# Performance work log

Hardware: AMD Instinct MI355X
Metric: run time of the kernel (lower is better)

## Reference

```python
import jax, jax.numpy as jnp
import numpy as np

B, H, W = 4, 112, 112
N = H * W              # 12544 tokens
NBHD = 48              # local neighborhood size
DIM = 256
OUT_DIM = 512
INNER = 4              # inner_ch of weight_net
TABLE = 4096           # pre_table rows
ALPHA = 4.0
DS_RATE = 0.25
STRIDE = 2
RESERVE = (H // 4) * (W // 4)  # 784 reserve tokens (pos % 4 == 0)
EPS = 1e-5


def _ln(x, g, b):
    m = x.mean(-1, keepdims=True)
    v = ((x - m) ** 2).mean(-1, keepdims=True)
    return (x - m) / jnp.sqrt(v + EPS) * g + b


def setup_inputs() -> dict:
    key = jax.random.key(0)
    ks = jax.random.split(key, 8)
    ii, jj = jnp.meshgrid(jnp.arange(H), jnp.arange(W), indexing='ij')
    pos = jnp.stack([ii, jj], -1).reshape(1, N, 2).astype(jnp.float32)
    pos = jnp.tile(pos, (B, 1, 1))                             # b x n x 2 integer grid
    feat = jax.random.normal(ks[0], (B, N, DIM), jnp.float32)
    member_idx = jax.random.randint(ks[1], (B, N, NBHD), 0, N)
    cluster_mask = (jax.random.uniform(ks[2], (B, N, NBHD)) > 0.1).astype(jnp.float32)
    learned_prob = jax.random.uniform(ks[3], (B, N, 1), dtype=jnp.float32)
    pe_idx = jax.random.randint(ks[4], (B, N, NBHD), 0, TABLE)
    pre_table = jax.random.normal(ks[5], (TABLE, 5), jnp.float32)
    w1 = jax.random.normal(ks[6], (5, INNER), jnp.float32) * 0.4
    b1 = jnp.zeros((INNER,), jnp.float32)
    ln1_g = jnp.ones((INNER,), jnp.float32)
    ln1_b = jnp.zeros((INNER,), jnp.float32)
    norm_g = jnp.ones((INNER * DIM,), jnp.float32)
    norm_b = jnp.zeros((INNER * DIM,), jnp.float32)
    lin_w = jax.random.normal(ks[7], (INNER * DIM, OUT_DIM), jnp.float32) * (1.0 / np.sqrt(INNER * DIM))
    lin_b = jnp.zeros((OUT_DIM,), jnp.float32)
    return dict(pos=pos, feat=feat, member_idx=member_idx, cluster_mask=cluster_mask,
                learned_prob=learned_prob, stride=STRIDE, pe_idx=pe_idx, reserve_num=RESERVE,
                pre_table=pre_table, w1=w1, b1=b1, ln1_g=ln1_g, ln1_b=ln1_b,
                norm_g=norm_g, norm_b=norm_b, lin_w=lin_w, lin_b=lin_b)


def reference(pos, feat, member_idx, cluster_mask, learned_prob, stride, pe_idx,
              reserve_num, pre_table, w1, b1, ln1_g, ln1_b, norm_g, norm_b, lin_w, lin_b):
    b, n, c = feat.shape
    keep_num = int(n * DS_RATE)
    pos_long = pos.astype(jnp.int32)
    # stride == 2 branch: tokens on the coarse grid get prob 1
    grid_prob = jnp.all(pos_long % stride == 0, axis=-1).astype(jnp.float32)      # b x n
    lp_s = jax.lax.stop_gradient(learned_prob).reshape(b, n) * ALPHA              # detached scores
    final_prob = grid_prob + lp_s
    reserve_mask = jnp.all(pos_long % (stride * 2) == 0, axis=-1).astype(jnp.float32)
    final_prob = final_prob + reserve_mask * (-100.0)
    sample_num = keep_num - reserve_num
    _, sample_idx = jax.lax.top_k(final_prob, sample_num)                         # b x sample_num
    # per-row nonzero of reserve_mask (exactly reserve_num hits per row)
    flat_nz = jnp.nonzero(reserve_mask.reshape(-1) > 0, size=b * reserve_num)[0]
    reserve_idx = (flat_nz % n).reshape(b, reserve_num).astype(sample_idx.dtype)
    idx = jnp.concatenate([sample_idx, reserve_idx], axis=1)                      # b x keep_num

    pos_k = jnp.take_along_axis(pos, idx[:, :, None], axis=1)                     # b x keep x 2
    nbhd = member_idx.shape[-1]
    mem_k = jnp.take_along_axis(member_idx, idx[:, :, None], axis=1)              # b x keep x nbhd
    pe_k = jnp.take_along_axis(pe_idx, idx[:, :, None], axis=1)
    cm_k = jnp.take_along_axis(cluster_mask, idx[:, :, None], axis=1)
    lp = jnp.take_along_axis(learned_prob, mem_k.reshape(b, -1, 1), axis=1)
    lp = lp.reshape(b, keep_num, nbhd, 1)

    # weight_net on the small PE table, then gather per-edge weights
    wt = jax.nn.gelu(_ln(pre_table @ w1 + b1, ln1_g, ln1_b), approximate=False)   # TABLE x INNER
    weights = wt[pe_k]                                                            # b x keep x nbhd x INNER
    weights = weights * (lp * cm_k[..., None])

    # CLUSTENWF: gather neighbor features and weighted-sum over the neighborhood
    gathered = jnp.take_along_axis(feat, mem_k.reshape(b, -1, 1), axis=1)
    gathered = gathered.reshape(b, keep_num, nbhd, c)                             # b x keep x nbhd x c
    out = jnp.einsum('bnkm,bnkc->bnmc', weights, gathered).reshape(b, keep_num, INNER * c)
    out = _ln(out, norm_g, norm_b)
    return pos_k, out @ lin_w + lin_b
```

## Files before the change

### kernel.cpp

```cpp
#include <hip/hip_runtime.h>

typedef unsigned short u16;
typedef unsigned int u32;
typedef unsigned long long u64;

#define NB 4
#define NTOK 12544
#define NBHD 48
#define DIM 256
#define OUTD 512
#define KEEPN 3136
#define SAMPLEN 2352
#define RESN 784
#define GW 112
#define POSN (NB * KEEPN * 2)
#define QTR (NTOK / 4)
#define NBKT 16384

#define BLKM 128
#define BLKN 256
#define BROW 40

#define FEATB_BYTES (25690112ull)
#define XWS_BYTES   (25690112ull)
#define LINT_BYTES  (1048576ull)
#define KEYS_BYTES  (401408ull)
#define PART_BYTES  (802816ull)
#define WS_NEED (FEATB_BYTES + XWS_BYTES + LINT_BYTES + KEYS_BYTES + PART_BYTES)

__device__ __forceinline__ float bf2f(u16 u) {
    union { u32 i; float f; } v; v.i = ((u32)u) << 16; return v.f;
}
__device__ __forceinline__ float asf(u32 u) {
    union { u32 i; float f; } v; v.i = u; return v.f;
}
__device__ __forceinline__ u16 f2bf(float f) {
    union { u32 i; float f; } v; v.f = f;
    return (u16)((v.i + 0x7FFFu + ((v.i >> 16) & 1u)) >> 16);
}

typedef __bf16 bf16x8 __attribute__((ext_vector_type(8)));
typedef float floatx4 __attribute__((ext_vector_type(4)));

__device__ __forceinline__ float make_f(float lp, int n) {
    int i = n / GW, j = n % GW;
    float f = lp * 4.0f;
    if (((i | j) & 1) == 0) f = 1.0f + f;
    if (((i | j) & 3) == 0) f = f + (-100.0f);
    return f;
}
__device__ __forceinline__ u64 f_to_key(float f, int n) {
    union { float f; u32 u; } v; v.f = f;
    u32 m = (v.u & 0x80000000u) ? ~v.u : (v.u | 0x80000000u);
    return (((u64)m) << 32) | (u64)(0xFFFFFFFFu - (u32)n);
}
__device__ __forceinline__ int f_to_bucket(float f) {
    int b = (int)floorf(f * 3276.8f);
    return b < 0 ? 0 : (b > NBKT - 1 ? NBKT - 1 : b);
}

__global__ __launch_bounds__(256) void feat_cvt_kernel(
    const float* __restrict__ feat, u16* __restrict__ featb) {
    int t = blockIdx.x * 256 + threadIdx.x;
    float4 v = ((const float4*)feat)[t];
    u64 w = (u64)f2bf(v.x) | ((u64)f2bf(v.y) << 16) |
            ((u64)f2bf(v.z) << 32) | ((u64)f2bf(v.w) << 48);
    ((u64*)featb)[t] = w;
}

__global__ __launch_bounds__(256) void linT_cvt_kernel(
    const float* __restrict__ lin_w, u16* __restrict__ linT,
    u32* __restrict__ hist) {
    __shared__ u16 T[64 * 65];
    int k0 = blockIdx.x * 64, n0 = blockIdx.y * 64;
    int t = threadIdx.x;
    int bid = blockIdx.y * 16 + blockIdx.x;
    hist[bid * 512 + t] = 0;
    hist[bid * 512 + 256 + t] = 0;
    int r = t >> 2, c4 = (t & 3) * 16;
#pragma unroll
    for (int i = 0; i < 4; ++i) {
        float4 v = *(const float4*)&lin_w[(size_t)(k0 + r) * OUTD + n0 + c4 + i * 4];
        T[(c4 + i * 4 + 0) * 65 + r] = f2bf(v.x);
        T[(c4 + i * 4 + 1) * 65 + r] = f2bf(v.y);
        T[(c4 + i * 4 + 2) * 65 + r] = f2bf(v.z);
        T[(c4 + i * 4 + 3) * 65 + r] = f2bf(v.w);
    }
    __syncthreads();
    int nl = t >> 2, kc = (t & 3) * 16;
    union { uint4 v[2]; u16 h[16]; } u;
#pragma unroll
    for (int i = 0; i < 16; ++i) u.h[i] = T[nl * 65 + kc + i];
    u16* dst = &linT[(size_t)(n0 + nl) * 1024 + k0 + kc];
    *(uint4*)(dst + 0) = u.v[0];
    *(uint4*)(dst + 8) = u.v[1];
}

__global__ __launch_bounds__(256) void hist_kernel(
    const float* __restrict__ lprob, u32* __restrict__ hist) {
    int g = blockIdx.x * 256 + threadIdx.x;
    int b = g / NTOK, n = g % NTOK;
    int bkt = f_to_bucket(make_f(lprob[g], n));
    atomicAdd(&hist[b * NBKT + bkt], 1u);
}

__global__ __launch_bounds__(1024) void prefix_kernel(
    const u32* __restrict__ hist, u32* __restrict__ base, u32* __restrict__ cursor) {
    int b = blockIdx.x, t = threadIdx.x;
    const u32* h = hist + b * NBKT;
    u32 loc[16], own = 0;
#pragma unroll
    for (int i = 0; i < 16; ++i) { loc[i] = h[t * 16 + i]; own += loc[i]; }
    __shared__ u32 buf[2][1024];
    buf[0][t] = own;
    __syncthreads();
    int src = 0;
    for (int off = 1; off < 1024; off <<= 1) {
        u32 v = buf[src][t] + ((t + off < 1024) ? buf[src][t + off] : 0u);
        buf[src ^ 1][t] = v;
        src ^= 1;
        __syncthreads();
    }
    u32 above = buf[src][t] - own;
    u32 suf = 0, bout[16];
    for (int i = 15; i >= 0; --i) { bout[i] = above + suf; suf += loc[i]; }
    u32* bb = base + b * NBKT;
    u32* cc = cursor + b * NBKT;
#pragma unroll
    for (int i = 0; i < 16; ++i) { bb[t * 16 + i] = bout[i]; cc[t * 16 + i] = bout[i]; }
}

__global__ __launch_bounds__(256) void scatter_kernel(
    const float* __restrict__ lprob, u32* __restrict__ cursor,
    u64* __restrict__ slots) {
    int g = blockIdx.x * 256 + threadIdx.x;
    int b = g / NTOK, n = g % NTOK;
    float f = make_f(lprob[g], n);
    int bkt = f_to_bucket(f);
    u32 s = atomicAdd(&cursor[b * NBKT + bkt], 1u);
    slots[b * NTOK + s] = f_to_key(f, n);
}

__global__ __launch_bounds__(256) void rank_finalize_kernel(
    const float* __restrict__ lprob, const u32* __restrict__ hist,
    const u32* __restrict__ base, const u64* __restrict__ slots,
    float* __restrict__ pos_out) {
    int g = blockIdx.x * 256 + threadIdx.x;
    int b = g / NTOK, n = g % NTOK;
    int i = n / GW, j = n % GW;
    if (((i | j) & 3) == 0) {
        int r = (i >> 2) * 28 + (j >> 2);
        int slot = b * KEEPN + SAMPLEN + r;
        pos_out[slot * 2 + 0] = (float)i;
        pos_out[slot * 2 + 1] = (float)j;
        return;
    }
    float f = make_f(lprob[g], n);
    int bkt = f_to_bucket(f);
    u32 r0 = base[b * NBKT + bkt];
    if (r0 >= SAMPLEN) return;
    u64 my = f_to_key(f, n);
    u32 cnt = hist[b * NBKT + bkt];
    const u64* sl = slots + b * NTOK + r0;
    u32 rank = r0;
    for (u32 s = 0; s < cnt; ++s) rank += (sl[s] > my) ? 1u : 0u;
    if (rank < SAMPLEN) {
        int slot = b * KEEPN + (int)rank;
        pos_out[slot * 2 + 0] = (float)i;
        pos_out[slot * 2 + 1] = (float)j;
    }
}

#define PSTR 20
__global__ __launch_bounds__(256) void token_v2_kernel(
    const float* __restrict__ pos_in, u16* __restrict__ xdst,
    const int* __restrict__ member_idx, const int* __restrict__ pe_idx,
    const float* __restrict__ cmask, const float* __restrict__ lprob,
    const u16* __restrict__ featb, const float* __restrict__ pre_table,
    const float* __restrict__ w1, const float* __restrict__ b1,
    const float* __restrict__ g1, const float* __restrict__ bb1,
    const float* __restrict__ norm_g, const float* __restrict__ norm_b) {
    int bi = blockIdx.x;
    int xcd = bi & 7, jj = bi >> 3;
    int b = xcd >> 1;
    int t = b * KEEPN + (xcd & 1) * 1568 + jj;
    int tid = threadIdx.x;
    int wave = tid >> 6, lane = tid & 63;
    __shared__ int mem_s[NBHD];
    __shared__ float4 w_s[NBHD];
    __shared__ float partials[4 * 64 * PSTR];
    __shared__ float red[10];

    int n_src = (int)pos_in[t * 2 + 0] * GW + (int)pos_in[t * 2 + 1];

    if (tid < NBHD) {
        int e = (b * NTOK + n_src) * NBHD + tid;
        int mem = member_idx[e];
        int pe = pe_idx[e];
        float cm = cmask[e];
        float lpe = lprob[b * NTOK + mem];
        float z[4];
#pragma unroll
        for (int m = 0; m < 4; ++m) {
            float acc = b1[m];
#pragma unroll
            for (int d = 0; d < 5; ++d) acc += pre_table[pe * 5 + d] * w1[d * 4 + m];
            z[m] = acc;
        }
        float mean = (z[0] + z[1] + z[2] + z[3]) * 0.25f;
        float var = 0.0f;
#pragma unroll
        for (int m = 0; m < 4; ++m) { float d = z[m] - mean; var += d * d; }
        float rstd = rsqrtf(var * 0.25f + 1e-5f);
        float sc = lpe * cm;
        float wv[4];
#pragma unroll
        for (int m = 0; m < 4; ++m) {
            float y = (z[m] - mean) * rstd * g1[m] + bb1[m];
            wv[m] = 0.5f * y * (1.0f + erff(y * 0.70710678118654752f)) * sc;
        }
        w_s[tid] = make_float4(wv[0], wv[1], wv[2], wv[3]);
        mem_s[tid] = mem;
    }
    __syncthreads();

    float acc[16];
#pragma unroll
    for (int i = 0; i < 16; ++i) acc[i] = 0.0f;
    const u16* fbase = featb + (size_t)b * NTOK * DIM + lane * 4;
    int k0 = wave * 12;
#pragma unroll
    for (int kk = 0; kk < 12; ++kk) {
        int k = k0 + kk;
        uint2 d = *(const uint2*)(fbase + (size_t)mem_s[k] * DIM);
        float4 w = w_s[k];
        float c0 = asf(d.x << 16);
        float c1 = asf(d.x & 0xFFFF0000u);
        float c2 = asf(d.y << 16);
        float c3 = asf(d.y & 0xFFFF0000u);
        acc[0]  += w.x * c0; acc[1]  += w.y * c0; acc[2]  += w.z * c0; acc[3]  += w.w * c0;
        acc[4]  += w.x * c1; acc[5]  += w.y * c1; acc[6]  += w.z * c1; acc[7]  += w.w * c1;
        acc[8]  += w.x * c2; acc[9]  += w.y * c2; acc[10] += w.z * c2; acc[11] += w.w * c2;
        acc[12] += w.x * c3; acc[13] += w.y * c3; acc[14] += w.z * c3; acc[15] += w.w * c3;
    }
    float* pp = &partials[(wave * 64 + lane) * PSTR];
#pragma unroll
    for (int i = 0; i < 4; ++i)
        *(float4*)(pp + i * 4) = make_float4(acc[i * 4], acc[i * 4 + 1],
                                             acc[i * 4 + 2], acc[i * 4 + 3]);
    __syncthreads();

    int c = tid;
    float a[4] = {0.f, 0.f, 0.f, 0.f};
#pragma unroll
    for (int w = 0; w < 4; ++w) {
        float4 v = *(const float4*)&partials[(w * 64 + (c >> 2)) * PSTR + (c & 3) * 4];
        a[0] += v.x; a[1] += v.y; a[2] += v.z; a[3] += v.w;
    }

    float s1 = a[0] + a[1] + a[2] + a[3];
    float s2 = a[0] * a[0] + a[1] * a[1] + a[2] * a[2] + a[3] * a[3];
#pragma unroll
    for (int off = 32; off > 0; off >>= 1) {
        s1 += __shfl_down(s1, off, 64);
        s2 += __shfl_down(s2, off, 64);
    }
    if (lane == 0) { red[wave] = s1; red[4 + wave] = s2; }
    __syncthreads();
    if (tid == 0) {
        float S = red[0] + red[1] + red[2] + red[3];
        float Q = red[4] + red[5] + red[6] + red[7];
        float mean = S * (1.0f / 1024.0f);
        float var = fmaxf(Q * (1.0f / 1024.0f) - mean * mean, 0.0f);
        red[8] = mean; red[9] = rsqrtf(var + 1e-5f);
    }
    __syncthreads();
    float mean = red[8], rstd = red[9];
    u16* Xp = xdst + (size_t)t * 1024;
#pragma unroll
    for (int m = 0; m < 4; ++m) {
        int cc = m * 256 + c;
        float v = (a[m] - mean) * rstd * norm_g[cc] + norm_b[cc];
        Xp[cc] = f2bf(v);
    }
}

#define GROW 40
__global__ __launch_bounds__(256) void gemm_tile_kernel(
    const u16* __restrict__ xws, const u16* __restrict__ linT,
    const float* __restrict__ lin_b, float* __restrict__ out) {
    __shared__ __align__(16) u16 As[128 * GROW];
    __shared__ __align__(16) u16 Bs[128 * GROW];
    int tid = threadIdx.x;
    int wave = tid >> 6, lane = tid & 63;
    int l15 = lane & 15, quad = lane >> 4;
    int wm = wave >> 1, wn = wave & 1;
    int m0 = blockIdx.x * 128, n0 = blockIdx.y * 128;
    int sr = tid >> 2, sk = (tid & 3) * 8;

    const u16* Ap0 = xws + (size_t)(m0 + sr) * 1024 + sk;
    const u16* Ap1 = Ap0 + (size_t)64 * 1024;
    const u16* Bp0 = linT + (size_t)(n0 + sr) * 1024 + sk;
    const u16* Bp1 = Bp0 + (size_t)64 * 1024;

    floatx4 acc[4][4] = {};
    for (int kk = 0; kk < 1024; kk += 32) {
        uint4 a0 = *(const uint4*)(Ap0 + kk);
        uint4 a1 = *(const uint4*)(Ap1 + kk);
        uint4 b0 = *(const uint4*)(Bp0 + kk);
        uint4 b1 = *(const uint4*)(Bp1 + kk);
        __syncthreads();
        *(uint4*)&As[sr * GROW + sk] = a0;
        *(uint4*)&As[(64 + sr) * GROW + sk] = a1;
        *(uint4*)&Bs[sr * GROW + sk] = b0;
        *(uint4*)&Bs[(64 + sr) * GROW + sk] = b1;
        __syncthreads();
        bf16x8 af[4], bfv[4];
#pragma unroll
        for (int mi = 0; mi < 4; ++mi)
            af[mi] = *(const bf16x8*)&As[(wm * 64 + mi * 16 + l15) * GROW + quad * 8];
#pragma unroll
        for (int ni = 0; ni < 4; ++ni)
            bfv[ni] = *(const bf16x8*)&Bs[(wn * 64 + ni * 16 + l15) * GROW + quad * 8];
#pragma unroll
        for (int mi = 0; mi < 4; ++mi)
#pragma unroll
            for (int ni = 0; ni < 4; ++ni)
                acc[mi][ni] = __builtin_amdgcn_mfma_f32_16x16x32_bf16(
                    af[mi], bfv[ni], acc[mi][ni], 0, 0, 0);
    }
#pragma unroll
    for (int ni = 0; ni < 4; ++ni) {
        int col = n0 + wn * 64 + ni * 16 + l15;
        float bias = lin_b[col];
#pragma unroll
        for (int mi = 0; mi < 4; ++mi)
#pragma unroll
            for (int reg = 0; reg < 4; ++reg) {
                int row = m0 + wm * 64 + mi * 16 + quad * 4 + reg;
                out[(size_t)row * OUTD + col] = acc[mi][ni][reg] + bias;
            }
    }
}

__global__ __launch_bounds__(256) void key_kernel(
    const float* __restrict__ lprob, u64* __restrict__ keys) {
    int g = blockIdx.x * 256 + threadIdx.x;
    int n = g % NTOK;
    keys[g] = f_to_key(make_f(lprob[g], n), n);
}

__global__ __launch_bounds__(256) void partial_rank_kernel(
    const u64* __restrict__ keys, u32* __restrict__ part) {
    int b = blockIdx.y, z = blockIdx.z;
    int n = blockIdx.x * 256 + threadIdx.x;
    u64 my = keys[b * NTOK + n];
    const u64* kb = keys + b * NTOK + z * QTR;
    u32 cnt = 0;
    for (int t = 0; t < QTR; t += 8) {
#pragma unroll
        for (int j = 0; j < 8; ++j) cnt += (kb[t + j] > my) ? 1u : 0u;
    }
    part[(z * NB + b) * NTOK + n] = cnt;
}

__global__ __launch_bounds__(256) void finalize_kernel(
    const u32* __restrict__ part, float* __restrict__ pos_out) {
    int b = blockIdx.y;
    int n = blockIdx.x * 256 + threadIdx.x;
    int g = b * NTOK + n;
    u32 rank = part[g] + part[(NB + b) * NTOK + n] +
               part[(2 * NB + b) * NTOK + n] + part[(3 * NB + b) * NTOK + n];
    int i = n / GW, j = n % GW;
    if (rank < SAMPLEN) {
        int slot = b * KEEPN + (int)rank;
        pos_out[slot * 2 + 0] = (float)i;
        pos_out[slot * 2 + 1] = (float)j;
    }
    if (((i | j) & 3) == 0) {
        int r = (i >> 2) * 28 + (j >> 2);
        int slot = b * KEEPN + SAMPLEN + r;
        pos_out[slot * 2 + 0] = (float)i;
        pos_out[slot * 2 + 1] = (float)j;
    }
}

__global__ __launch_bounds__(256) void token_fb_kernel(
    const float* __restrict__ pos_in, u16* __restrict__ xdst,
    const int* __restrict__ member_idx, const int* __restrict__ pe_idx,
    const float* __restrict__ cmask, const float* __restrict__ lprob,
    const float* __restrict__ featf, const float* __restrict__ pre_table,
    const float* __restrict__ w1, const float* __restrict__ b1,
    const float* __restrict__ g1, const float* __restrict__ bb1,
    const float* __restrict__ norm_g, const float* __restrict__ norm_b) {
    int t = blockIdx.x;
    int b = t / KEEPN;
    int tid = threadIdx.x;
    __shared__ int mem_s[NBHD];
    __shared__ float4 w_s[NBHD];
    __shared__ float red[10];

    int n_src = (int)pos_in[t * 2 + 0] * GW + (int)pos_in[t * 2 + 1];

    if (tid < NBHD) {
        int e = (b * NTOK + n_src) * NBHD + tid;
        int mem = member_idx[e];
        int pe = pe_idx[e];
        float cm = cmask[e];
        float lpe = lprob[b * NTOK + mem];
        float z[4];
#pragma unroll
        for (int m = 0; m < 4; ++m) {
            float acc = b1[m];
#pragma unroll
            for (int d = 0; d < 5; ++d) acc += pre_table[pe * 5 + d] * w1[d * 4 + m];
            z[m] = acc;
        }
        float mean = (z[0] + z[1] + z[2] + z[3]) * 0.25f;
        float var = 0.0f;
#pragma unroll
        for (int m = 0; m < 4; ++m) { float d = z[m] - mean; var += d * d; }
        float rstd = rsqrtf(var * 0.25f + 1e-5f);
        float sc = lpe * cm;
        float wv[4];
#pragma unroll
        for (int m = 0; m < 4; ++m) {
            float y = (z[m] - mean) * rstd * g1[m] + bb1[m];
            wv[m] = 0.5f * y * (1.0f + erff(y * 0.70710678118654752f)) * sc;
        }
        w_s[tid] = make_float4(wv[0], wv[1], wv[2], wv[3]);
        mem_s[tid] = mem;
    }
    __syncthreads();

    float a0 = 0.f, a1 = 0.f, a2 = 0.f, a3 = 0.f;
    size_t base = (size_t)b * NTOK * DIM + tid;
#pragma unroll 8
    for (int k = 0; k < NBHD; ++k) {
        float g = featf[base + (size_t)mem_s[k] * DIM];
        float4 w = w_s[k];
        a0 += w.x * g; a1 += w.y * g; a2 += w.z * g; a3 += w.w * g;
    }
    float s1 = a0 + a1 + a2 + a3;
    float s2 = a0 * a0 + a1 * a1 + a2 * a2 + a3 * a3;
#pragma unroll
    for (int off = 32; off > 0; off >>= 1) {
        s1 += __shfl_down(s1, off, 64);
        s2 += __shfl_down(s2, off, 64);
    }
    int wave = tid >> 6, lane = tid & 63;
    if (lane == 0) { red[wave] = s1; red[4 + wave] = s2; }
    __syncthreads();
    if (tid == 0) {
        float S = red[0] + red[1] + red[2] + red[3];
        float Q = red[4] + red[5] + red[6] + red[7];
        float mean = S * (1.0f / 1024.0f);
        float var = fmaxf(Q * (1.0f / 1024.0f) - mean * mean, 0.0f);
        red[8] = mean; red[9] = rsqrtf(var + 1e-5f);
    }
    __syncthreads();
    float mean = red[8], rstd = red[9];
    float acc4[4] = {a0, a1, a2, a3};
    u16* Xp = xdst + (size_t)t * 1024;
#pragma unroll
    for (int m = 0; m < 4; ++m) {
        int cc = m * 256 + tid;
        float v = (acc4[m] - mean) * rstd * norm_g[cc] + norm_b[cc];
        Xp[cc] = f2bf(v);
    }
}

__global__ __launch_bounds__(256) void gemm_inplace_kernel(
    const float* __restrict__ lin_w, const float* __restrict__ lin_b,
    float* __restrict__ out) {
    __shared__ __align__(16) u16 Bs[BLKN * BROW];
    int tile_m = blockIdx.x;
    int nblk = blockIdx.y;
    int tid = threadIdx.x;
    int wave = tid >> 6, lane = tid & 63;
    int l15 = lane & 15, quad = lane >> 4;

    const u16* Xbase = (const u16*)out;
    floatx4 acc[8][4] = {};

    for (int kk = 0; kk < 1024; kk += 32) {
        __syncthreads();
#pragma unroll
        for (int it = 0; it < 4; ++it) {
            int task = it * 256 + tid;
            int kp = task >> 6;
            int ng = task & 63;
            int k = kp * 2;
            int n0 = nblk * BLKN + ng * 4;
            float4 fa = *(const float4*)&lin_w[(size_t)(kk + k) * OUTD + n0];
            float4 fb = *(const float4*)&lin_w[(size_t)(kk + k + 1) * OUTD + n0];
            u16* bp = &Bs[(ng * 4) * BROW + k];
            *(u32*)(bp + 0 * BROW) = (u32)f2bf(fa.x) | ((u32)f2bf(fb.x) << 16);
            *(u32*)(bp + 1 * BROW) = (u32)f2bf(fa.y) | ((u32)f2bf(fb.y) << 16);
            *(u32*)(bp + 2 * BROW) = (u32)f2bf(fa.z) | ((u32)f2bf(fb.z) << 16);
            *(u32*)(bp + 3 * BROW) = (u32)f2bf(fa.w) | ((u32)f2bf(fb.w) << 16);
        }
        __syncthreads();
        bf16x8 bfrag[4];
#pragma unroll
        for (int ni = 0; ni < 4; ++ni)
            bfrag[ni] = *(const bf16x8*)&Bs[(wave * 64 + ni * 16 + l15) * BROW + quad * 8];
#pragma unroll
        for (int mi = 0; mi < 8; ++mi) {
            int row = tile_m * BLKM + mi * 16 + l15;
            bf16x8 af = *(const bf16x8*)&Xbase[(size_t)row * 1024 + kk + quad * 8];
#pragma unroll
            for (int ni = 0; ni < 4; ++ni)
                acc[mi][ni] = __builtin_amdgcn_mfma_f32_16x16x32_bf16(
                    af, bfrag[ni], acc[mi][ni], 0, 0, 0);
        }
    }
    __syncthreads();
#pragma unroll
    for (int mi = 0; mi < 8; ++mi)
#pragma unroll
        for (int ni = 0; ni < 4; ++ni) {
            int col = nblk * BLKN + wave * 64 + ni * 16 + l15;
            float bias = lin_b[col];
#pragma unroll
            for (int reg = 0; reg < 4; ++reg) {
                int row = tile_m * BLKM + mi * 16 + quad * 4 + reg;
                out[(size_t)row * OUTD + col] = acc[mi][ni][reg] + bias;
            }
        }
}

extern "C" void kernel_launch(void* const* d_in, const int* in_sizes, int n_in,
                              void* d_out, int out_size, void* d_ws, size_t ws_size,
                              hipStream_t stream) {
    const float* feat     = (const float*)d_in[1];
    const int* member_idx = (const int*)d_in[2];
    const float* cmask    = (const float*)d_in[3];
    const float* lprob    = (const float*)d_in[4];
    const int* pe_idx     = (const int*)d_in[6];
    const float* pre_table= (const float*)d_in[8];
    const float* w1       = (const float*)d_in[9];
    const float* b1       = (const float*)d_in[10];
    const float* g1       = (const float*)d_in[11];
    const float* bb1      = (const float*)d_in[12];
    const float* norm_g   = (const float*)d_in[13];
    const float* norm_b   = (const float*)d_in[14];
    const float* lin_w    = (const float*)d_in[15];
    const float* lin_b    = (const float*)d_in[16];

    float* pos_out = (float*)d_out;
    float* out     = pos_out + POSN;

    if (ws_size >= WS_NEED) {
        char* ws = (char*)d_ws;
        u16* featb = (u16*)ws;
        u16* xws   = (u16*)(ws + FEATB_BYTES);
        u16* linT  = (u16*)(ws + FEATB_BYTES + XWS_BYTES);
        u64* slots = (u64*)(ws + FEATB_BYTES + XWS_BYTES + LINT_BYTES);
        u32* hist  = (u32*)(ws + FEATB_BYTES + XWS_BYTES + LINT_BYTES + KEYS_BYTES);
        u32* base  = hist + NB * NBKT;
        u32* curs  = base + NB * NBKT;

        feat_cvt_kernel<<<12544, 256, 0, stream>>>(feat, featb);
        linT_cvt_kernel<<<dim3(16, 8), 256, 0, stream>>>(lin_w, linT, hist);
        hist_kernel<<<(NB * NTOK) / 256, 256, 0, stream>>>(lprob, hist);
        prefix_kernel<<<NB, 1024, 0, stream>>>(hist, base, curs);
        scatter_kernel<<<(NB * NTOK) / 256, 256, 0, stream>>>(lprob, curs, slots);
        rank_finalize_kernel<<<(NB * NTOK) / 256, 256, 0, stream>>>(
            lprob, hist, base, slots, pos_out);
        token_v2_kernel<<<NB * KEEPN, 256, 0, stream>>>(
            pos_out, xws, member_idx, pe_idx, cmask, lprob, featb,
            pre_table, w1, b1, g1, bb1, norm_g, norm_b);
        gemm_tile_kernel<<<dim3(98, 4), 256, 0, stream>>>(xws, linT, lin_b, out);
    } else {
        u64* keys = (u64*)out;
        u32* part = (u32*)((char*)out + 401408);

        key_kernel<<<(NB * NTOK) / 256, 256, 0, stream>>>(lprob, keys);
        partial_rank_kernel<<<dim3(49, NB, 4), 256, 0, stream>>>(keys, part);
        finalize_kernel<<<dim3(49, NB), 256, 0, stream>>>(part, pos_out);
        token_fb_kernel<<<NB * KEEPN, 256, 0, stream>>>(
            pos_out, (u16*)out, member_idx, pe_idx, cmask, lprob, feat,
            pre_table, w1, b1, g1, bb1, norm_g, norm_b);
        gemm_inplace_kernel<<<dim3(98, 2), 256, 0, stream>>>(lin_w, lin_b, out);
    }
}
```

Measured before the change: 254.1 us.

## Split token aggregation into weight-table, channel-tiled gather, and separate LayerNorm kernels

```diff
diff --git a/kernel.cpp b/kernel.cpp
--- a/kernel.cpp
+++ b/kernel.cpp
@@ -21,18 +21,20 @@
 #define BLKN 256
 #define BROW 40
 
-#define FEATB_BYTES (25690112ull)
 #define XWS_BYTES   (25690112ull)
+#define WTAB_BYTES  (9633792ull)
 #define LINT_BYTES  (1048576ull)
-#define KEYS_BYTES  (401408ull)
-#define PART_BYTES  (802816ull)
-#define WS_NEED (FEATB_BYTES + XWS_BYTES + LINT_BYTES + KEYS_BYTES + PART_BYTES)
+#define SLOTS_BYTES (401408ull)
+#define PART_BYTES  (786432ull)
+#define XWS_OFF   0ull
+#define WTAB_OFF  (XWS_OFF + XWS_BYTES)
+#define LINT_OFF  (WTAB_OFF + WTAB_BYTES)
+#define SLOTS_OFF (LINT_OFF + LINT_BYTES)
+#define HIST_OFF  (SLOTS_OFF + SLOTS_BYTES)
+#define WS_NEED   (HIST_OFF + PART_BYTES)
 
 __device__ __forceinline__ float bf2f(u16 u) {
     union { u32 i; float f; } v; v.i = ((u32)u) << 16; return v.f;
-}
-__device__ __forceinline__ float asf(u32 u) {
-    union { u32 i; float f; } v; v.i = u; return v.f;
 }
 __device__ __forceinline__ u16 f2bf(float f) {
     union { u32 i; float f; } v; v.f = f;
@@ -57,15 +59,6 @@
 __device__ __forceinline__ int f_to_bucket(float f) {
     int b = (int)floorf(f * 3276.8f);
     return b < 0 ? 0 : (b > NBKT - 1 ? NBKT - 1 : b);
-}
-
-__global__ __launch_bounds__(256) void feat_cvt_kernel(
-    const float* __restrict__ feat, u16* __restrict__ featb) {
-    int t = blockIdx.x * 256 + threadIdx.x;
-    float4 v = ((const float4*)feat)[t];
-    u64 w = (u64)f2bf(v.x) | ((u64)f2bf(v.y) << 16) |
-            ((u64)f2bf(v.z) << 32) | ((u64)f2bf(v.w) << 48);
-    ((u64*)featb)[t] = w;
 }
 
 __global__ __launch_bounds__(256) void linT_cvt_kernel(
@@ -171,95 +164,116 @@
     }
 }
 
-#define PSTR 20
-__global__ __launch_bounds__(256) void token_v2_kernel(
-    const float* __restrict__ pos_in, u16* __restrict__ xdst,
-    const int* __restrict__ member_idx, const int* __restrict__ pe_idx,
-    const float* __restrict__ cmask, const float* __restrict__ lprob,
-    const u16* __restrict__ featb, const float* __restrict__ pre_table,
+__global__ __launch_bounds__(256) void wtab_kernel(
+    const float* __restrict__ pos_in, const int* __restrict__ member_idx,
+    const int* __restrict__ pe_idx, const float* __restrict__ cmask,
+    const float* __restrict__ lprob, const float* __restrict__ pre_table,
     const float* __restrict__ w1, const float* __restrict__ b1,
     const float* __restrict__ g1, const float* __restrict__ bb1,
-    const float* __restrict__ norm_g, const float* __restrict__ norm_b) {
-    int bi = blockIdx.x;
-    int xcd = bi & 7, jj = bi >> 3;
+    float4* __restrict__ wtab) {
+    int g = blockIdx.x * 256 + threadIdx.x;
+    int t = g / NBHD, k = g - t * NBHD;
+    int b = t / KEEPN;
+    int n_src = (int)pos_in[t * 2 + 0] * GW + (int)pos_in[t * 2 + 1];
+    int e = (b * NTOK + n_src) * NBHD + k;
+    int mem = member_idx[e];
+    int pe = pe_idx[e];
+    float cm = cmask[e];
+    float lpe = lprob[b * NTOK + mem];
+    float z[4];
+#pragma unroll
+    for (int m = 0; m < 4; ++m) {
+        float acc = b1[m];
+#pragma unroll
+        for (int d = 0; d < 5; ++d) acc += pre_table[pe * 5 + d] * w1[d * 4 + m];
+        z[m] = acc;
+    }
+    float mean = (z[0] + z[1] + z[2] + z[3]) * 0.25f;
+    float var = 0.0f;
+#pragma unroll
+    for (int m = 0; m < 4; ++m) { float d = z[m] - mean; var += d * d; }
+    float rstd = rsqrtf(var * 0.25f + 1e-5f);
+    float sc = lpe * cm;
+    float wv[4];
+#pragma unroll
+    for (int m = 0; m < 4; ++m) {
+        float y = (z[m] - mean) * rstd * g1[m] + bb1[m];
+        wv[m] = 0.5f * y * (1.0f + erff(y * 0.70710678118654752f)) * sc;
+    }
+    wtab[g] = make_float4(wv[0], wv[1], wv[2], wv[3]);
+}
+
+__global__ __launch_bounds__(256) void token_v4_kernel(
+    const float* __restrict__ pos_in, const float4* __restrict__ wtab,
+    const int* __restrict__ member_idx, const float* __restrict__ feat,
+    u16* __restrict__ xws) {
+    __shared__ int nsrc_s[16];
+    __shared__ int mem_s[16][NBHD];
+    __shared__ __align__(16) float4 w_s[16][NBHD];
+
+    int x = blockIdx.x;
+    int xcd = x & 7, j = x >> 3;
     int b = xcd >> 1;
-    int t = b * KEEPN + (xcd & 1) * 1568 + jj;
+    int t0 = b * KEEPN + ((xcd & 1) * 98 + j) * 16;
+    int tile = blockIdx.y;
+    int ch0 = tile * 32;
     int tid = threadIdx.x;
     int wave = tid >> 6, lane = tid & 63;
-    __shared__ int mem_s[NBHD];
-    __shared__ float4 w_s[NBHD];
-    __shared__ float partials[4 * 64 * PSTR];
+    int r4 = lane >> 4, cp = lane & 15;
+
+    if (tid < 16)
+        nsrc_s[tid] = (int)pos_in[(t0 + tid) * 2 + 0] * GW +
+                      (int)pos_in[(t0 + tid) * 2 + 1];
+    __syncthreads();
+#pragma unroll
+    for (int e = tid; e < 16 * NBHD; e += 256) {
+        int tok = e / NBHD, k = e - tok * NBHD;
+        mem_s[tok][k] = member_idx[(b * NTOK + nsrc_s[tok]) * NBHD + k];
+        ((float4*)w_s)[e] = wtab[(t0 + tok) * NBHD + k];
+    }
+    __syncthreads();
+
+    const float* fb = feat + (size_t)b * NTOK * DIM + ch0 + cp * 2;
+#pragma unroll
+    for (int tt = 0; tt < 4; ++tt) {
+        int tok = wave * 4 + tt;
+        float a[8] = {0.f, 0.f, 0.f, 0.f, 0.f, 0.f, 0.f, 0.f};
+#pragma unroll
+        for (int i = 0; i < 12; ++i) {
+            int row = i * 4 + r4;
+            int mem = mem_s[tok][row];
+            float4 w = w_s[tok][row];
+            float2 g = *(const float2*)(fb + (size_t)mem * DIM);
+            a[0] += w.x * g.x; a[1] += w.y * g.x; a[2] += w.z * g.x; a[3] += w.w * g.x;
+            a[4] += w.x * g.y; a[5] += w.y * g.y; a[6] += w.z * g.y; a[7] += w.w * g.y;
+        }
+#pragma unroll
+        for (int i = 0; i < 8; ++i) {
+            a[i] += __shfl_xor(a[i], 16, 64);
+            a[i] += __shfl_xor(a[i], 32, 64);
+        }
+        if (r4 == 0) {
+            u16* X = xws + (size_t)(t0 + tok) * 1024 + ch0 + cp * 2;
+#pragma unroll
+            for (int m = 0; m < 4; ++m)
+                *(u32*)(X + m * 256) = (u32)f2bf(a[m]) | ((u32)f2bf(a[4 + m]) << 16);
+        }
+    }
+}
+
+__global__ __launch_bounds__(256) void ln_kernel(
+    u16* __restrict__ xws, const float* __restrict__ norm_g,
+    const float* __restrict__ norm_b) {
+    int t = blockIdx.x;
+    int tid = threadIdx.x;
+    int wave = tid >> 6, lane = tid & 63;
     __shared__ float red[10];
-
-    int n_src = (int)pos_in[t * 2 + 0] * GW + (int)pos_in[t * 2 + 1];
-
-    if (tid < NBHD) {
-        int e = (b * NTOK + n_src) * NBHD + tid;
-        int mem = member_idx[e];
-        int pe = pe_idx[e];
-        float cm = cmask[e];
-        float lpe = lprob[b * NTOK + mem];
-        float z[4];
-#pragma unroll
-        for (int m = 0; m < 4; ++m) {
-            float acc = b1[m];
-#pragma unroll
-            for (int d = 0; d < 5; ++d) acc += pre_table[pe * 5 + d] * w1[d * 4 + m];
-            z[m] = acc;
-        }
-        float mean = (z[0] + z[1] + z[2] + z[3]) * 0.25f;
-        float var = 0.0f;
-#pragma unroll
-        for (int m = 0; m < 4; ++m) { float d = z[m] - mean; var += d * d; }
-        float rstd = rsqrtf(var * 0.25f + 1e-5f);
-        float sc = lpe * cm;
-        float wv[4];
-#pragma unroll
-        for (int m = 0; m < 4; ++m) {
-            float y = (z[m] - mean) * rstd * g1[m] + bb1[m];
-            wv[m] = 0.5f * y * (1.0f + erff(y * 0.70710678118654752f)) * sc;
-        }
-        w_s[tid] = make_float4(wv[0], wv[1], wv[2], wv[3]);
-        mem_s[tid] = mem;
-    }
-    __syncthreads();
-
-    float acc[16];
-#pragma unroll
-    for (int i = 0; i < 16; ++i) acc[i] = 0.0f;
-    const u16* fbase = featb + (size_t)b * NTOK * DIM + lane * 4;
-    int k0 = wave * 12;
-#pragma unroll
-    for (int kk = 0; kk < 12; ++kk) {
-        int k = k0 + kk;
-        uint2 d = *(const uint2*)(fbase + (size_t)mem_s[k] * DIM);
-        float4 w = w_s[k];
-        float c0 = asf(d.x << 16);
-        float c1 = asf(d.x & 0xFFFF0000u);
-        float c2 = asf(d.y << 16);
-        float c3 = asf(d.y & 0xFFFF0000u);
-        acc[0]  += w.x * c0; acc[1]  += w.y * c0; acc[2]  += w.z * c0; acc[3]  += w.w * c0;
-        acc[4]  += w.x * c1; acc[5]  += w.y * c1; acc[6]  += w.z * c1; acc[7]  += w.w * c1;
-        acc[8]  += w.x * c2; acc[9]  += w.y * c2; acc[10] += w.z * c2; acc[11] += w.w * c2;
-        acc[12] += w.x * c3; acc[13] += w.y * c3; acc[14] += w.z * c3; acc[15] += w.w * c3;
-    }
-    float* pp = &partials[(wave * 64 + lane) * PSTR];
-#pragma unroll
-    for (int i = 0; i < 4; ++i)
-        *(float4*)(pp + i * 4) = make_float4(acc[i * 4], acc[i * 4 + 1],
-                                             acc[i * 4 + 2], acc[i * 4 + 3]);
-    __syncthreads();
-
-    int c = tid;
-    float a[4] = {0.f, 0.f, 0.f, 0.f};
-#pragma unroll
-    for (int w = 0; w < 4; ++w) {
-        float4 v = *(const float4*)&partials[(w * 64 + (c >> 2)) * PSTR + (c & 3) * 4];
-        a[0] += v.x; a[1] += v.y; a[2] += v.z; a[3] += v.w;
-    }
-
-    float s1 = a[0] + a[1] + a[2] + a[3];
-    float s2 = a[0] * a[0] + a[1] * a[1] + a[2] * a[2] + a[3] * a[3];
+    u16* X = xws + (size_t)t * 1024;
+    union { u64 w; u16 h[4]; } d;
+    d.w = *(const u64*)(X + tid * 4);
+    float v0 = bf2f(d.h[0]), v1 = bf2f(d.h[1]), v2 = bf2f(d.h[2]), v3 = bf2f(d.h[3]);
+    float s1 = v0 + v1 + v2 + v3;
+    float s2 = v0 * v0 + v1 * v1 + v2 * v2 + v3 * v3;
 #pragma unroll
     for (int off = 32; off > 0; off >>= 1) {
         s1 += __shfl_down(s1, off, 64);
@@ -276,13 +290,14 @@
     }
     __syncthreads();
     float mean = red[8], rstd = red[9];
-    u16* Xp = xdst + (size_t)t * 1024;
-#pragma unroll
-    for (int m = 0; m < 4; ++m) {
-        int cc = m * 256 + c;
-        float v = (a[m] - mean) * rstd * norm_g[cc] + norm_b[cc];
-        Xp[cc] = f2bf(v);
-    }
+    float4 g = *(const float4*)&norm_g[tid * 4];
+    float4 bb = *(const float4*)&norm_b[tid * 4];
+    union { u64 w; u16 h[4]; } o;
+    o.h[0] = f2bf((v0 - mean) * rstd * g.x + bb.x);
+    o.h[1] = f2bf((v1 - mean) * rstd * g.y + bb.y);
+    o.h[2] = f2bf((v2 - mean) * rstd * g.z + bb.z);
+    o.h[3] = f2bf((v3 - mean) * rstd * g.w + bb.w);
+    *(u64*)(X + tid * 4) = o.w;
 }
 
 #define GROW 40
@@ -295,7 +310,7 @@
     int wave = tid >> 6, lane = tid & 63;
     int l15 = lane & 15, quad = lane >> 4;
     int wm = wave >> 1, wn = wave & 1;
-    int m0 = blockIdx.x * 128, n0 = blockIdx.y * 128;
+    int m0 = blockIdx.y * 128, n0 = blockIdx.x * 128;
     int sr = tid >> 2, sk = (tid & 3) * 8;
 
     const u16* Ap0 = xws + (size_t)(m0 + sr) * 1024 + sk;
@@ -553,25 +568,27 @@
 
     if (ws_size >= WS_NEED) {
         char* ws = (char*)d_ws;
-        u16* featb = (u16*)ws;
-        u16* xws   = (u16*)(ws + FEATB_BYTES);
-        u16* linT  = (u16*)(ws + FEATB_BYTES + XWS_BYTES);
-        u64* slots = (u64*)(ws + FEATB_BYTES + XWS_BYTES + LINT_BYTES);
-        u32* hist  = (u32*)(ws + FEATB_BYTES + XWS_BYTES + LINT_BYTES + KEYS_BYTES);
-        u32* base  = hist + NB * NBKT;
-        u32* curs  = base + NB * NBKT;
-
-        feat_cvt_kernel<<<12544, 256, 0, stream>>>(feat, featb);
+        u16*    xws   = (u16*)(ws + XWS_OFF);
+        float4* wtab  = (float4*)(ws + WTAB_OFF);
+        u16*    linT  = (u16*)(ws + LINT_OFF);
+        u64*    slots = (u64*)(ws + SLOTS_OFF);
+        u32*    hist  = (u32*)(ws + HIST_OFF);
+        u32*    base  = hist + NB * NBKT;
+        u32*    curs  = base + NB * NBKT;
+
         linT_cvt_kernel<<<dim3(16, 8), 256, 0, stream>>>(lin_w, linT, hist);
         hist_kernel<<<(NB * NTOK) / 256, 256, 0, stream>>>(lprob, hist);
         prefix_kernel<<<NB, 1024, 0, stream>>>(hist, base, curs);
         scatter_kernel<<<(NB * NTOK) / 256, 256, 0, stream>>>(lprob, curs, slots);
         rank_finalize_kernel<<<(NB * NTOK) / 256, 256, 0, stream>>>(
             lprob, hist, base, slots, pos_out);
-        token_v2_kernel<<<NB * KEEPN, 256, 0, stream>>>(
-            pos_out, xws, member_idx, pe_idx, cmask, lprob, featb,
-            pre_table, w1, b1, g1, bb1, norm_g, norm_b);
-        gemm_tile_kernel<<<dim3(98, 4), 256, 0, stream>>>(xws, linT, lin_b, out);
+        wtab_kernel<<<(NB * KEEPN * NBHD) / 256, 256, 0, stream>>>(
+            pos_out, member_idx, pe_idx, cmask, lprob, pre_table,
+            w1, b1, g1, bb1, wtab);
+        token_v4_kernel<<<dim3(784, 8), 256, 0, stream>>>(
+            pos_out, wtab, member_idx, feat, xws);
+        ln_kernel<<<NB * KEEPN, 256, 0, stream>>>(xws, norm_g, norm_b);
+        gemm_tile_kernel<<<dim3(4, 98), 256, 0, stream>>>(xws, linT, lin_b, out);
     } else {
         u64* keys = (u64*)out;
         u32* part = (u32*)((char*)out + 401408);
```

Result: slower. 279.7 us (+10.1%).
